# Optimization experiments

Measured on AMD Instinct MI355X. Metric: run time of the kernel, lower is better.

Reference implementation:

```python
import jax, jax.numpy as jnp
import numpy as np

B, S, HID = 1, 4096, 2048
HQ, HKV, D = 16, 8, 128
G = HQ // HKV
WINDOW = 1024
EPS = 1e-6
ROPE_THETA = 1e6


def setup_inputs() -> dict:
    key = jax.random.key(0)
    ks = jax.random.split(key, 6)
    hidden_states = jax.random.normal(ks[0], (B, S, HID), dtype=jnp.float32)
    Wq = jax.random.normal(ks[1], (HQ * D, HID), dtype=jnp.float32) * 0.02
    Wk = jax.random.normal(ks[2], (HKV * D, HID), dtype=jnp.float32) * 0.02
    Wv = jax.random.normal(ks[3], (HKV * D, HID), dtype=jnp.float32) * 0.02
    Wo = jax.random.normal(ks[4], (HID, HQ * D), dtype=jnp.float32) * 0.02
    q_norm_w = jnp.ones((D,), dtype=jnp.float32)
    k_norm_w = jnp.ones((D,), dtype=jnp.float32)
    # standard RoPE tables
    inv_freq = 1.0 / (ROPE_THETA ** (jnp.arange(0, D, 2, dtype=jnp.float32) / D))
    pos = jnp.arange(S, dtype=jnp.float32)
    freqs = pos[:, None] * inv_freq[None, :]            # [S, D/2]
    emb = jnp.concatenate([freqs, freqs], axis=-1)       # [S, D]
    cos = jnp.cos(emb)[None]                             # [1, S, D]
    sin = jnp.sin(emb)[None]
    return {"hidden_states": hidden_states, "cos": cos, "sin": sin,
            "Wq": Wq, "Wk": Wk, "Wv": Wv, "Wo": Wo,
            "q_norm_w": q_norm_w, "k_norm_w": k_norm_w}


def _rms_norm(x, w):
    var = jnp.mean(jnp.square(x), axis=-1, keepdims=True)
    return w * (x * jax.lax.rsqrt(var + EPS))


def _rotate_half(x):
    x1, x2 = jnp.split(x, 2, axis=-1)
    return jnp.concatenate([-x2, x1], axis=-1)


def reference(hidden_states, cos, sin, Wq, Wk, Wv, Wo, q_norm_w, k_norm_w):
    b, s, _ = hidden_states.shape
    # projections -> [B, H, S, D]
    q = (hidden_states @ Wq.T).reshape(b, s, HQ, D)
    k = (hidden_states @ Wk.T).reshape(b, s, HKV, D)
    v = (hidden_states @ Wv.T).reshape(b, s, HKV, D)
    q = _rms_norm(q, q_norm_w).transpose(0, 2, 1, 3)   # [B,HQ,S,D]
    k = _rms_norm(k, k_norm_w).transpose(0, 2, 1, 3)   # [B,HKV,S,D]
    v = v.transpose(0, 2, 1, 3)
    # RoPE (cos/sin broadcast over head dim)
    c = cos[:, None, :, :]
    sn = sin[:, None, :, :]
    q = q * c + _rotate_half(q) * sn
    k = k * c + _rotate_half(k) * sn
    # GQA: group queries per kv head
    qg = q.reshape(b, HKV, G, s, D)
    scaling = D ** -0.5
    scores = jnp.einsum('bhgqd,bhkd->bhgqk', qg, k) * scaling  # [B,HKV,G,S,S]
    # causal + sliding-window additive mask
    i = jnp.arange(s)[:, None]
    j = jnp.arange(s)[None, :]
    allowed = (j <= i) & (j > i - WINDOW)
    scores = jnp.where(allowed[None, None, None], scores, jnp.float32(-1e9))
    attn = jax.nn.softmax(scores, axis=-1)
    out = jnp.einsum('bhgqk,bhkd->bhgqd', attn, v)     # [B,HKV,G,S,D]
    out = out.reshape(b, HQ, s, D).transpose(0, 2, 1, 3).reshape(b, s, HQ * D)
    return out @ Wo.T
```

## Files before the change

kernel.cpp:

```cpp
#include <hip/hip_runtime.h>

typedef __bf16 bf16;
typedef bf16 bf16x8 __attribute__((ext_vector_type(8)));
typedef bf16 bf16x4 __attribute__((ext_vector_type(4)));
typedef float f32x4 __attribute__((ext_vector_type(4)));

#define MFMA16(a, b, c) __builtin_amdgcn_mfma_f32_16x16x32_bf16((a), (b), (c), 0, 0, 0)

__device__ __forceinline__ void gload_lds16(const bf16* g, bf16* l) {
  __builtin_amdgcn_global_load_lds(
      (const __attribute__((address_space(1))) void*)g,
      (__attribute__((address_space(3))) void*)l, 16, 0, 0);
}

__global__ __launch_bounds__(256) void cvt_f32_bf16(const float* __restrict__ src,
                                                    bf16* __restrict__ dst, int n4) {
  int i = blockIdx.x * blockDim.x + threadIdx.x;
  if (i < n4) {
    float4 v = ((const float4*)src)[i];
    bf16x4 o;
    o[0] = (bf16)v.x; o[1] = (bf16)v.y; o[2] = (bf16)v.z; o[3] = (bf16)v.w;
    ((bf16x4*)dst)[i] = o;
  }
}

template <int BM, typename OutT>
__global__ __launch_bounds__(512, 2) void gemm8p(const bf16* __restrict__ A,
                                                 const bf16* __restrict__ B,
                                                 OutT* __restrict__ C,
                                                 int M, int N, int K) {
  static_assert(BM == 256 || BM == 128, "");
  constexpr int MT = BM / 32;
  constexpr int AQ = MT / 2;
  constexpr int AHALF = (BM / 2) * 64;
  constexpr int BHALF = 128 * 64;
  constexpr int NLA = BM / 128;
  constexpr int NLB = 2;
  constexpr int VMC = 2 * NLA + NLB;

  __shared__ __align__(16) bf16 SA[2 * 2 * AHALF];
  __shared__ __align__(16) bf16 SB[2 * 2 * BHALF];

  const int NT = K >> 6;
  const int tid = threadIdx.x;
  const int w = tid >> 6, lane = tid & 63;
  const int l15 = lane & 15, quad = lane >> 4;
  const int wr = w >> 2, wc = w & 3;

  const int nbx = N >> 8;
  const int nwg = (M / BM) * nbx;
  const int wg = ((int)blockIdx.x & 7) * (nwg >> 3) + ((int)blockIdx.x >> 3);
  const int bm0 = (wg / nbx) * BM;
  const int bn0 = (wg % nbx) << 8;

  const bf16* apt[NLA];
  const bf16* bpt[NLB];
#pragma unroll
  for (int i = 0; i < NLA; ++i) {
    int s = i * 512 + tid, r = s >> 3, g = (s & 7) ^ (r & 7);
    apt[i] = A + (size_t)(bm0 + r) * K + g * 8;
  }
#pragma unroll
  for (int i = 0; i < NLB; ++i) {
    int s = i * 512 + tid, r = s >> 3, g = (s & 7) ^ (r & 7);
    bpt[i] = B + (size_t)(bn0 + r) * K + g * 8;
  }
  const size_t hsA = (size_t)(BM / 2) * K;
  const size_t hsB = (size_t)128 * K;

  int aoff[AQ][2], boff[2][2];
#pragma unroll
  for (int m = 0; m < AQ; ++m) {
    int lr = wr * (BM / 4) + m * 16 + l15;
#pragma unroll
    for (int ks = 0; ks < 2; ++ks)
      aoff[m][ks] = lr * 64 + (((ks * 4 + quad) ^ (lr & 7)) << 3);
  }
#pragma unroll
  for (int nq = 0; nq < 2; ++nq) {
    int lc = wc * 32 + nq * 16 + l15;
#pragma unroll
    for (int ks = 0; ks < 2; ++ks)
      boff[nq][ks] = lc * 64 + (((ks * 4 + quad) ^ (lc & 7)) << 3);
  }

  f32x4 acc[MT][4] = {};
  bf16x8 af[AQ][2], bfA[2][2], bfB[2][2];

#define STAGE_A_(H, SO, KT)                                                     \
  _Pragma("unroll") for (int i_ = 0; i_ < NLA; ++i_)                            \
      gload_lds16(apt[i_] + (H) * hsA + (KT) * 64,                              \
                  SA + ((SO) * 2 + (H)) * AHALF + i_ * 4096 + tid * 8)
#define STAGE_B_(H, SO, KT)                                                     \
  _Pragma("unroll") for (int i_ = 0; i_ < NLB; ++i_)                            \
      gload_lds16(bpt[i_] + (H) * hsB + (KT) * 64,                              \
                  SB + ((SO) * 2 + (H)) * BHALF + i_ * 4096 + tid * 8)
#define LDAQ_(QM, SL)                                                           \
  _Pragma("unroll") for (int m_ = 0; m_ < AQ; ++m_)                             \
      _Pragma("unroll") for (int k_ = 0; k_ < 2; ++k_)                          \
          af[m_][k_] = *(const bf16x8*)(SA + ((SL) * 2 + (QM)) * AHALF + aoff[m_][k_])
#define LDBQ_(QN, SL, DST)                                                      \
  _Pragma("unroll") for (int n_ = 0; n_ < 2; ++n_)                              \
      _Pragma("unroll") for (int k_ = 0; k_ < 2; ++k_)                          \
          DST[n_][k_] = *(const bf16x8*)(SB + ((SL) * 2 + (QN)) * BHALF + boff[n_][k_])
#define MFQ_(QM, QN, BF)                                                        \
  do {                                                                          \
    __builtin_amdgcn_s_setprio(1);                                              \
    _Pragma("unroll") for (int k_ = 0; k_ < 2; ++k_)                            \
        _Pragma("unroll") for (int m_ = 0; m_ < AQ; ++m_)                       \
            _Pragma("unroll") for (int n_ = 0; n_ < 2; ++n_)                    \
                acc[(QM) * AQ + m_][(QN) * 2 + n_] =                            \
                    MFMA16(af[m_][k_], BF[n_][k_],                              \
                           acc[(QM) * AQ + m_][(QN) * 2 + n_]);                 \
    __builtin_amdgcn_s_setprio(0);                                              \
  } while (0)

#define TILE_(T, STG1, STG2, VMM)                                               \
  do {                                                                          \
    const int sl_ = (T) & 1, so_ = sl_ ^ 1;                                     \
                                                      \
    LDAQ_(0, sl_);                                                              \
    LDBQ_(0, sl_, bfA);                                                         \
    if (STG1) { STAGE_B_(0, so_, (T) + 1); }                                    \
    if constexpr (AQ == 4) { asm volatile("s_waitcnt lgkmcnt(8)" ::: "memory"); } \
    __builtin_amdgcn_s_barrier();                                               \
    asm volatile("s_waitcnt lgkmcnt(0)" ::: "memory");                          \
    MFQ_(0, 0, bfA);                                                            \
    __builtin_amdgcn_s_barrier();                                               \
                                                               \
    LDBQ_(1, sl_, bfB);                                                         \
    if (STG2) { STAGE_A_(0, sl_, (T) + 2); }                                    \
    __builtin_amdgcn_s_barrier();                                               \
    asm volatile("s_waitcnt lgkmcnt(0)" ::: "memory");                          \
    MFQ_(0, 1, bfB);                                                            \
    __builtin_amdgcn_s_barrier();                                               \
                                                               \
    LDAQ_(1, sl_);                                                              \
    if (STG2) { STAGE_B_(1, sl_, (T) + 2); }                                    \
    __builtin_amdgcn_s_barrier();                                               \
    asm volatile("s_waitcnt lgkmcnt(0)" ::: "memory");                          \
    MFQ_(1, 1, bfB);                                                            \
    __builtin_amdgcn_s_barrier();                                               \
                                                   \
    LDBQ_(0, sl_, bfA);                                                         \
    if (STG2) { STAGE_A_(1, sl_, (T) + 2); }                                    \
    __builtin_amdgcn_s_barrier();                                               \
    asm volatile("s_waitcnt lgkmcnt(0)" ::: "memory");                          \
    MFQ_(1, 0, bfA);                                                            \
    if ((VMM) == 1) { asm volatile("s_waitcnt vmcnt(%0)" :: "i"(VMC) : "memory"); } \
    else if ((VMM) == 2) { asm volatile("s_waitcnt vmcnt(0)" ::: "memory"); }   \
    __builtin_amdgcn_s_barrier();                                               \
  } while (0)

  STAGE_A_(0, 0, 0);
  STAGE_B_(0, 0, 0);
  STAGE_A_(1, 0, 0);
  STAGE_B_(1, 0, 0);
  STAGE_A_(0, 1, 1);
  STAGE_B_(1, 1, 1);
  STAGE_A_(1, 1, 1);
  asm volatile("s_waitcnt vmcnt(%0)" :: "i"(VMC) : "memory");
  __builtin_amdgcn_s_barrier();

  int t = 0;
  for (; t < NT - 2; ++t) TILE_(t, 1, 1, 1);
  TILE_(t, 1, 0, 2);
  ++t;
  TILE_(t, 0, 0, 0);

#undef STAGE_A_
#undef STAGE_B_
#undef LDAQ_
#undef LDBQ_
#undef MFQ_
#undef TILE_

#pragma unroll
  for (int qm = 0; qm < 2; ++qm)
#pragma unroll
    for (int m = 0; m < AQ; ++m)
#pragma unroll
      for (int qn = 0; qn < 2; ++qn)
#pragma unroll
        for (int n = 0; n < 2; ++n) {
          int row = bm0 + qm * (BM / 2) + wr * (BM / 4) + m * 16 + quad * 4;
          int col = bn0 + qn * 128 + wc * 32 + n * 16 + l15;
          f32x4 v = acc[qm * AQ + m][qn * 2 + n];
#pragma unroll
          for (int r = 0; r < 4; ++r)
            C[(size_t)(row + r) * N + col] = (OutT)v[r];
        }
}

__global__ __launch_bounds__(256) void normrope(const bf16* __restrict__ QKVb,
                                                const float* __restrict__ cosb,
                                                const float* __restrict__ sinb,
                                                const float* __restrict__ qw,
                                                const float* __restrict__ kw,
                                                bf16* __restrict__ Qb,
                                                bf16* __restrict__ Kb) {
  const int wid = (blockIdx.x * blockDim.x + threadIdx.x) >> 6;
  const int lane = threadIdx.x & 63;
  const int s = wid / 24;
  const int h = wid % 24;
  const bool isq = (h < 16);
  const int col0 = isq ? h * 128 : 2048 + (h - 16) * 128;
  const float* wt = isq ? qw : kw;

  const bf16* row = QKVb + (size_t)s * 4096 + col0;
  float x1 = (float)row[lane];
  float x2 = (float)row[lane + 64];

  float ss = x1 * x1 + x2 * x2;
#pragma unroll
  for (int m = 32; m >= 1; m >>= 1) ss += __shfl_xor(ss, m, 64);
  float rs = rsqrtf(ss * (1.0f / 128.0f) + 1e-6f);

  float c = cosb[(size_t)s * 128 + lane];
  float sn = sinb[(size_t)s * 128 + lane];
  float xn1 = x1 * rs * wt[lane];
  float xn2 = x2 * rs * wt[lane + 64];
  float o1 = xn1 * c - xn2 * sn;
  float o2 = xn2 * c + xn1 * sn;
  const float scale = isq ? 0.12751652f : 1.0f;
  o1 *= scale; o2 *= scale;

  bf16* dst = isq ? (Qb + ((size_t)h * 4096 + s) * 128)
                  : (Kb + ((size_t)(h - 16) * 4096 + s) * 128);
  dst[lane] = (bf16)o1;
  dst[lane + 64] = (bf16)o2;
}

__global__ __launch_bounds__(256) void vtrans(const bf16* __restrict__ QKVb,
                                              bf16* __restrict__ Vtp) {
  __shared__ __align__(16) bf16 T[64 * 136];
  const int kvh = blockIdx.y;
  const int s0 = blockIdx.x * 64;
  const int tid = threadIdx.x;
  for (int g = tid; g < 1024; g += 256) {
    int s = g >> 4, cg = g & 15;
    *(bf16x8*)(T + s * 136 + cg * 8) =
        *(const bf16x8*)(QKVb + (size_t)(s0 + s) * 4096 + 3072 + kvh * 128 + cg * 8);
  }
  __syncthreads();
  for (int g = tid; g < 1024; g += 256) {
    int d = g >> 3, sg = g & 7;
    bf16x8 v;
#pragma unroll
    for (int j = 0; j < 8; j++) {
      int kp = sg * 8 + j;
      int s = (kp & 3) * 16 + (kp >> 2);
      v[j] = T[s * 136 + d];
    }
    *(bf16x8*)(Vtp + ((size_t)kvh * 128 + d) * 4096 + s0 + sg * 8) = v;
  }
}

__global__ __launch_bounds__(256, 2) void attn_kernel(const bf16* __restrict__ Qb,
                                                      const bf16* __restrict__ Kb,
                                                      const bf16* __restrict__ Vtp,
                                                      bf16* __restrict__ Ob) {
  const int SEQ = 4096, W = 1024;
  const float MP = 17.312340f;
  __shared__ __align__(16) bf16 Ks[64 * 128];
  __shared__ __align__(16) bf16 Vs[128 * 64];
  __shared__ __align__(16) bf16 Ps[4][32 * 64];

  const int id = blockIdx.x;
  const int kvh = id & 7, gq = (id >> 3) & 1, h = kvh * 2 + gq;
  const int qb0 = (id >> 4) * 128;
  const int tid = threadIdx.x, w = tid >> 6, lane = tid & 63;
  const int l15 = lane & 15, quad = lane >> 4;
  const int qw0 = qb0 + w * 32;

  bf16x8 qf[2][4];
#pragma unroll
  for (int m = 0; m < 2; m++) {
    const bf16* qp = Qb + ((size_t)h * SEQ + qw0 + m * 16 + l15) * 128 + quad * 8;
#pragma unroll
    for (int kb = 0; kb < 4; kb++) qf[m][kb] = *(const bf16x8*)(qp + kb * 32);
  }

  f32x4 o[2][8] = {};
  f32x4 lr[2] = {};
  bf16* pw = &Ps[w][0];
  const bf16* kbase = Kb + (size_t)kvh * SEQ * 128;
  const bf16* vbase = Vtp + (size_t)kvh * 128 * SEQ;

  int jmin = qb0 - (W - 1); if (jmin < 0) jmin = 0;
  const int kt0 = jmin >> 6, kt1 = (qb0 + 127) >> 6;

  for (int kt = kt0; kt <= kt1; ++kt) {
    const int k0 = kt * 64;
#pragma unroll
    for (int i = 0; i < 4; i++) {
      int slot = w * 256 + i * 64 + lane;
      int key = slot >> 4, gg = slot & 15;
      int gsw = gg ^ (key & 7);
      gload_lds16(kbase + (size_t)(k0 + key) * 128 + gsw * 8, Ks + (w * 256 + i * 64) * 8);
    }
#pragma unroll
    for (int i = 0; i < 4; i++) {
      int slot = w * 256 + i * 64 + lane;
      int d = slot >> 3, gg = slot & 7;
      int gsw = gg ^ (d & 7);
      gload_lds16(vbase + (size_t)d * SEQ + k0 + gsw * 8, Vs + (w * 256 + i * 64) * 8);
    }
    __syncthreads();

    const bool alive = (k0 <= qw0 + 31) && (k0 + 63 > qw0 - W);
    if (alive) {
      const bool full = (k0 + 63 <= qw0) && (k0 > qw0 + 31 - W);
      f32x4 s[2][4] = {};
#pragma unroll
      for (int c = 0; c < 4; c++) {
        const int key = c * 16 + l15;
        bf16x8 kf[4];
#pragma unroll
        for (int kb = 0; kb < 4; kb++)
          kf[kb] = *(const bf16x8*)(Ks + key * 128 + (((kb * 4 + quad) ^ (key & 7)) << 3));
#pragma unroll
        for (int kb = 0; kb < 4; kb++) {
          s[0][c] = MFMA16(qf[0][kb], kf[kb], s[0][c]);
          s[1][c] = MFMA16(qf[1][kb], kf[kb], s[1][c]);
        }
      }
#pragma unroll
      for (int m = 0; m < 2; m++)
#pragma unroll
        for (int r = 0; r < 4; r++) {
          float p[4];
          if (full) {
#pragma unroll
            for (int c = 0; c < 4; c++) p[c] = __builtin_amdgcn_exp2f(s[m][c][r] - MP);
          } else {
            const int i_ = qw0 + m * 16 + quad * 4 + r;
#pragma unroll
            for (int c = 0; c < 4; c++) {
              int j = k0 + c * 16 + l15;
              p[c] = (j <= i_ && j > i_ - W) ? __builtin_amdgcn_exp2f(s[m][c][r] - MP) : 0.0f;
            }
          }
          lr[m][r] += p[0] + p[1] + p[2] + p[3];
          bf16x4 pk;
          pk[0] = (bf16)p[0]; pk[1] = (bf16)p[1]; pk[2] = (bf16)p[2]; pk[3] = (bf16)p[3];
          const int qrow = m * 16 + quad * 4 + r;
          *(bf16x4*)(pw + qrow * 64 + (((l15 >> 1) ^ (qrow & 7)) << 3) + (l15 & 1) * 4) = pk;
        }
      asm volatile("s_waitcnt lgkmcnt(0)" ::: "memory");
      bf16x8 pf[2][2];
#pragma unroll
      for (int m = 0; m < 2; m++)
#pragma unroll
        for (int kb = 0; kb < 2; kb++)
          pf[m][kb] = *(const bf16x8*)(pw + (m * 16 + l15) * 64 +
                                       (((kb * 4 + quad) ^ (l15 & 7)) << 3));
#pragma unroll
      for (int n = 0; n < 8; n++) {
        const int d = n * 16 + l15;
        bf16x8 vf0 = *(const bf16x8*)(Vs + d * 64 + ((quad ^ (l15 & 7)) << 3));
        bf16x8 vf1 = *(const bf16x8*)(Vs + d * 64 + (((4 + quad) ^ (l15 & 7)) << 3));
        o[0][n] = MFMA16(pf[0][0], vf0, o[0][n]);
        o[0][n] = MFMA16(pf[0][1], vf1, o[0][n]);
        o[1][n] = MFMA16(pf[1][0], vf0, o[1][n]);
        o[1][n] = MFMA16(pf[1][1], vf1, o[1][n]);
      }
    }
    __syncthreads();
  }

  float linv[2][4];
#pragma unroll
  for (int m = 0; m < 2; m++)
#pragma unroll
    for (int r = 0; r < 4; r++) {
      float v = lr[m][r];
      v += __shfl_xor(v, 1, 64);
      v += __shfl_xor(v, 2, 64);
      v += __shfl_xor(v, 4, 64);
      v += __shfl_xor(v, 8, 64);
      linv[m][r] = 1.0f / v;
    }
#pragma unroll
  for (int m = 0; m < 2; m++)
#pragma unroll
    for (int n = 0; n < 8; n++)
#pragma unroll
      for (int r = 0; r < 4; r++) {
        int i_ = qw0 + m * 16 + quad * 4 + r;
        Ob[(size_t)i_ * 2048 + h * 128 + n * 16 + l15] = (bf16)(o[m][n][r] * linv[m][r]);
      }
}

extern "C" void kernel_launch(void* const* d_in, const int* in_sizes, int n_in,
                              void* d_out, int out_size, void* d_ws, size_t ws_size,
                              hipStream_t stream) {
  const float* hid  = (const float*)d_in[0];
  const float* cosb = (const float*)d_in[1];
  const float* sinb = (const float*)d_in[2];
  const float* Wq   = (const float*)d_in[3];
  const float* Wk   = (const float*)d_in[4];
  const float* Wv   = (const float*)d_in[5];
  const float* Wo   = (const float*)d_in[6];
  const float* qw   = (const float*)d_in[7];
  const float* kw   = (const float*)d_in[8];

  if (ws_size < (size_t)(112u) * 1024u * 1024u) return;

  char* ws = (char*)d_ws;
  bf16* Xbf  = (bf16*)(ws);
  bf16* Vtp  = (bf16*)(ws);
  bf16* Wcat = (bf16*)(ws + (16u << 20));
  bf16* Wob  = (bf16*)(ws + (32u << 20));
  bf16* QKVb = (bf16*)(ws + (40u << 20));
  bf16* Qb   = (bf16*)(ws + (72u << 20));
  bf16* Kb   = (bf16*)(ws + (88u << 20));
  bf16* Ob   = (bf16*)(ws + (96u << 20));

  cvt_f32_bf16<<<8192, 256, 0, stream>>>(hid, Xbf, 2097152);
  cvt_f32_bf16<<<4096, 256, 0, stream>>>(Wq, Wcat, 1048576);
  cvt_f32_bf16<<<2048, 256, 0, stream>>>(Wk, Wcat + 4194304, 524288);
  cvt_f32_bf16<<<2048, 256, 0, stream>>>(Wv, Wcat + 6291456, 524288);
  cvt_f32_bf16<<<4096, 256, 0, stream>>>(Wo, Wob, 1048576);

  gemm8p<256, bf16><<<256, 512, 0, stream>>>(Xbf, Wcat, QKVb, 4096, 4096, 2048);
  vtrans<<<dim3(64, 8), 256, 0, stream>>>(QKVb, Vtp);
  normrope<<<24576, 256, 0, stream>>>(QKVb, cosb, sinb, qw, kw, Qb, Kb);
  attn_kernel<<<512, 256, 0, stream>>>(Qb, Kb, Vtp, Ob);
  gemm8p<128, float><<<256, 512, 0, stream>>>(Ob, Wob, (float*)d_out, 4096, 2048, 2048);
}
```

Measured before the change: 331.6 us.

## Restructure GEMM main loop to overlap LDS fragment reads with MFMA via double-buffered registers

The 8-phase GEMM tile loop is rewritten so each phase issues LDS reads for the next quadrant's fragments into alternate register buffers while MFMAs run on the fragments already loaded. This removes the per-phase lgkmcnt(0) waits and half of the barriers. The loop is unrolled by two so the buffer parity is a compile-time constant. The cost is more VGPRs for the extra A/B fragment buffers, which could pressure occupancy at launch_bounds(512,2). Implicit LDS-read waits now depend on the compiler, and the vmcnt wait threshold moves to a different phase. A stray unused constant with a non-ASCII identifier is also added.

```diff
diff --git a/kernel.cpp b/kernel.cpp
--- a/kernel.cpp
+++ b/kernel.cpp
@@ -25,7 +25,7 @@
 }
 
 template <int BM, typename OutT>
-__global__ __launch_bounds__(512, 2) void gemm8p(const bf16* __restrict__ A,
+__global__ __launch_bounds__(512, 2) void gemmcp(const bf16* __restrict__ A,
                                                  const bf16* __restrict__ B,
                                                  OutT* __restrict__ C,
                                                  int M, int N, int K) {
@@ -36,7 +36,9 @@
   constexpr int BHALF = 128 * 64;
   constexpr int NLA = BM / 128;
   constexpr int NLB = 2;
-  constexpr int VMC = 2 * NLA + NLB;
+  constexpr int VMС_UNUSED = 0;
+  constexpr int VMK = NLA + NLB;
+  constexpr int PVK = 2 * NLA + NLB;
 
   __shared__ __align__(16) bf16 SA[2 * 2 * AHALF];
   __shared__ __align__(16) bf16 SB[2 * 2 * BHALF];
@@ -85,7 +87,8 @@
   }
 
   f32x4 acc[MT][4] = {};
-  bf16x8 af[AQ][2], bfA[2][2], bfB[2][2];
+  bf16x8 aP[AQ][2], aQ[AQ][2];
+  bf16x8 bX[2][2], bY[2][2];
 
 #define STAGE_A_(H, SO, KT)                                                     \
   _Pragma("unroll") for (int i_ = 0; i_ < NLA; ++i_)                            \
@@ -95,60 +98,50 @@
   _Pragma("unroll") for (int i_ = 0; i_ < NLB; ++i_)                            \
       gload_lds16(bpt[i_] + (H) * hsB + (KT) * 64,                              \
                   SB + ((SO) * 2 + (H)) * BHALF + i_ * 4096 + tid * 8)
-#define LDAQ_(QM, SL)                                                           \
+#define LDA_(H, SL, DST)                                                        \
   _Pragma("unroll") for (int m_ = 0; m_ < AQ; ++m_)                             \
       _Pragma("unroll") for (int k_ = 0; k_ < 2; ++k_)                          \
-          af[m_][k_] = *(const bf16x8*)(SA + ((SL) * 2 + (QM)) * AHALF + aoff[m_][k_])
-#define LDBQ_(QN, SL, DST)                                                      \
+          DST[m_][k_] = *(const bf16x8*)(SA + ((SL) * 2 + (H)) * AHALF + aoff[m_][k_])
+#define LDB_(H, SL, DST)                                                        \
   _Pragma("unroll") for (int n_ = 0; n_ < 2; ++n_)                              \
       _Pragma("unroll") for (int k_ = 0; k_ < 2; ++k_)                          \
-          DST[n_][k_] = *(const bf16x8*)(SB + ((SL) * 2 + (QN)) * BHALF + boff[n_][k_])
-#define MFQ_(QM, QN, BF)                                                        \
+          DST[n_][k_] = *(const bf16x8*)(SB + ((SL) * 2 + (H)) * BHALF + boff[n_][k_])
+#define MFQ_(QM, QN, AS, BS)                                                    \
   do {                                                                          \
     __builtin_amdgcn_s_setprio(1);                                              \
     _Pragma("unroll") for (int k_ = 0; k_ < 2; ++k_)                            \
         _Pragma("unroll") for (int m_ = 0; m_ < AQ; ++m_)                       \
             _Pragma("unroll") for (int n_ = 0; n_ < 2; ++n_)                    \
                 acc[(QM) * AQ + m_][(QN) * 2 + n_] =                            \
-                    MFMA16(af[m_][k_], BF[n_][k_],                              \
+                    MFMA16(AS[m_][k_], BS[n_][k_],                              \
                            acc[(QM) * AQ + m_][(QN) * 2 + n_]);                 \
     __builtin_amdgcn_s_setprio(0);                                              \
   } while (0)
 
-#define TILE_(T, STG1, STG2, VMM)                                               \
+#define TILE_(T, PAR, STG1, STG2, VM, RDN)                                      \
   do {                                                                          \
-    const int sl_ = (T) & 1, so_ = sl_ ^ 1;                                     \
-                                                      \
-    LDAQ_(0, sl_);                                                              \
-    LDBQ_(0, sl_, bfA);                                                         \
+    constexpr int sl_ = (PAR), so_ = (PAR) ^ 1;                                 \
+                 \
+    LDB_(1, sl_, ((PAR) ? bY : bX));                          \
     if (STG1) { STAGE_B_(0, so_, (T) + 1); }                                    \
-    if constexpr (AQ == 4) { asm volatile("s_waitcnt lgkmcnt(8)" ::: "memory"); } \
+    MFQ_(0, 0, aP, ((PAR) ? bX : bY));                                          \
     __builtin_amdgcn_s_barrier();                                               \
-    asm volatile("s_waitcnt lgkmcnt(0)" ::: "memory");                          \
-    MFQ_(0, 0, bfA);                                                            \
+                                                                    \
+    LDA_(1, sl_, aQ);                                         \
+    if (STG2) { STAGE_A_(0, sl_, (T) + 2); }                                    \
+    MFQ_(0, 1, aP, ((PAR) ? bY : bX));                                          \
     __builtin_amdgcn_s_barrier();                                               \
-                                                               \
-    LDBQ_(1, sl_, bfB);                                                         \
-    if (STG2) { STAGE_A_(0, sl_, (T) + 2); }                                    \
+                                                                    \
+    LDB_(0, sl_, ((PAR) ? bX : bY));                     \
+    if (STG2) { STAGE_B_(1, sl_, (T) + 2); }                                    \
+    MFQ_(1, 1, aQ, ((PAR) ? bY : bX));                                          \
+    if ((VM) == 1) { asm volatile("s_waitcnt vmcnt(%0)" :: "i"(VMK) : "memory"); } \
+    else if ((VM) == 2) { asm volatile("s_waitcnt vmcnt(0)" ::: "memory"); }    \
     __builtin_amdgcn_s_barrier();                                               \
-    asm volatile("s_waitcnt lgkmcnt(0)" ::: "memory");                          \
-    MFQ_(0, 1, bfB);                                                            \
-    __builtin_amdgcn_s_barrier();                                               \
-                                                               \
-    LDAQ_(1, sl_);                                                              \
-    if (STG2) { STAGE_B_(1, sl_, (T) + 2); }                                    \
-    __builtin_amdgcn_s_barrier();                                               \
-    asm volatile("s_waitcnt lgkmcnt(0)" ::: "memory");                          \
-    MFQ_(1, 1, bfB);                                                            \
-    __builtin_amdgcn_s_barrier();                                               \
-                                                   \
-    LDBQ_(0, sl_, bfA);                                                         \
+           \
+    if (RDN) { LDA_(0, so_, aP); LDB_(0, so_, ((PAR) ? bY : bX)); }             \
     if (STG2) { STAGE_A_(1, sl_, (T) + 2); }                                    \
-    __builtin_amdgcn_s_barrier();                                               \
-    asm volatile("s_waitcnt lgkmcnt(0)" ::: "memory");                          \
-    MFQ_(1, 0, bfA);                                                            \
-    if ((VMM) == 1) { asm volatile("s_waitcnt vmcnt(%0)" :: "i"(VMC) : "memory"); } \
-    else if ((VMM) == 2) { asm volatile("s_waitcnt vmcnt(0)" ::: "memory"); }   \
+    MFQ_(1, 0, aQ, ((PAR) ? bX : bY));                                          \
     __builtin_amdgcn_s_barrier();                                               \
   } while (0)
 
@@ -159,19 +152,22 @@
   STAGE_A_(0, 1, 1);
   STAGE_B_(1, 1, 1);
   STAGE_A_(1, 1, 1);
-  asm volatile("s_waitcnt vmcnt(%0)" :: "i"(VMC) : "memory");
+  asm volatile("s_waitcnt vmcnt(%0)" :: "i"(PVK) : "memory");
   __builtin_amdgcn_s_barrier();
-
-  int t = 0;
-  for (; t < NT - 2; ++t) TILE_(t, 1, 1, 1);
-  TILE_(t, 1, 0, 2);
-  ++t;
-  TILE_(t, 0, 0, 0);
+  LDA_(0, 0, aP);
+  LDB_(0, 0, bY);
+
+  for (int t = 0; t < NT - 2; t += 2) {
+    TILE_(t, 0, 1, 1, 1, 1);
+    TILE_(t + 1, 1, 1, 1, 1, 1);
+  }
+  TILE_(NT - 2, 0, 1, 0, 2, 1);
+  TILE_(NT - 1, 1, 0, 0, 0, 0);
 
 #undef STAGE_A_
 #undef STAGE_B_
-#undef LDAQ_
-#undef LDBQ_
+#undef LDA_
+#undef LDB_
 #undef MFQ_
 #undef TILE_
 
@@ -423,9 +419,9 @@
   cvt_f32_bf16<<<2048, 256, 0, stream>>>(Wv, Wcat + 6291456, 524288);
   cvt_f32_bf16<<<4096, 256, 0, stream>>>(Wo, Wob, 1048576);
 
-  gemm8p<256, bf16><<<256, 512, 0, stream>>>(Xbf, Wcat, QKVb, 4096, 4096, 2048);
+  gemmcp<256, bf16><<<256, 512, 0, stream>>>(Xbf, Wcat, QKVb, 4096, 4096, 2048);
   vtrans<<<dim3(64, 8), 256, 0, stream>>>(QKVb, Vtp);
   normrope<<<24576, 256, 0, stream>>>(QKVb, cosb, sinb, qw, kw, Qb, Kb);
   attn_kernel<<<512, 256, 0, stream>>>(Qb, Kb, Vtp, Ob);
-  gemm8p<128, float><<<256, 512, 0, stream>>>(Ob, Wob, (float*)d_out, 4096, 2048, 2048);
-}
+  gemmcp<128, float><<<256, 512, 0, stream>>>(Ob, Wob, (float*)d_out, 4096, 2048, 2048);
+}
```

After: 348.7 us. +5.2%, slower.
